# Performance work log

Hardware: AMD Instinct MI355X
Metric: run time of the kernel (lower is better)

## Reference

```python
import jax, jax.numpy as jnp
import numpy as np

B, S, N, C, D = 1, 6, 6400, 128, 4
HEADS, POINTS = 4, 20
HS, WS = 32, 88
M = HS * WS
DH = C // HEADS


def setup_inputs() -> dict:
    key = jax.random.key(0)
    ks = jax.random.split(key, 16)
    sc = 0.02
    return {
        "query": jax.random.normal(ks[0], (B, N, C), jnp.float32),
        "key": jax.random.normal(ks[1], (S, M, B, C), jnp.float32),
        "value": jax.random.normal(ks[2], (S, M, B, C), jnp.float32),
        "query_pos": jax.random.normal(ks[3], (B, N, C), jnp.float32),
        "reference_points_cam": jax.random.uniform(ks[4], (S, B, N, D, 2), jnp.float32),
        "bev_mask": jax.random.bernoulli(ks[5], 0.3, (S, B, N, D)),
        "spatial_shapes": jnp.array([[HS, WS]], jnp.int32),
        "level_start_index": jnp.zeros((1,), jnp.int32),
        "Wv": sc * jax.random.normal(ks[6], (C, C), jnp.float32),
        "bv": jnp.zeros((C,), jnp.float32),
        "Woff": sc * jax.random.normal(ks[7], (C, HEADS * POINTS * 2), jnp.float32),
        "boff": sc * jax.random.normal(ks[8], (HEADS * POINTS * 2,), jnp.float32),
        "Wattn": sc * jax.random.normal(ks[9], (C, HEADS * POINTS), jnp.float32),
        "battn": jnp.zeros((HEADS * POINTS,), jnp.float32),
        "Wout": sc * jax.random.normal(ks[10], (C, C), jnp.float32),
        "bout": jnp.zeros((C,), jnp.float32),
    }


def _bilinear(img, x, y):
    # img: (G, HS, WS, DH); x, y: (G, Q, P) pixel coords (grid_sample align_corners=False, zero padding)
    G = img.shape[0]
    flat = img.reshape(G, HS * WS, DH)
    x0 = jnp.floor(x)
    y0 = jnp.floor(y)
    wx1 = x - x0
    wy1 = y - y0
    x0i = x0.astype(jnp.int32)
    y0i = y0.astype(jnp.int32)

    def gather(xi, yi):
        valid = ((xi >= 0) & (xi < WS) & (yi >= 0) & (yi < HS)).astype(img.dtype)
        idx = jnp.clip(yi, 0, HS - 1) * WS + jnp.clip(xi, 0, WS - 1)
        v = jnp.take_along_axis(flat, idx.reshape(G, -1, 1), axis=1)
        return v.reshape(*idx.shape, DH) * valid[..., None]

    v00 = gather(x0i, y0i)
    v01 = gather(x0i + 1, y0i)
    v10 = gather(x0i, y0i + 1)
    v11 = gather(x0i + 1, y0i + 1)
    return (v00 * ((1 - wx1) * (1 - wy1))[..., None]
            + v01 * (wx1 * (1 - wy1))[..., None]
            + v10 * ((1 - wx1) * wy1)[..., None]
            + v11 * (wx1 * wy1)[..., None])


def _deform_attn(q, v, ref, spatial_shapes, Wv, bv, Woff, boff, Wattn, battn):
    # q: (bs, nq, C); v: (bs, M, C); ref: (bs, nq, D, 2) in [0,1]
    bs, nq, _ = q.shape
    val = (v @ Wv + bv).reshape(bs, HS, WS, HEADS, DH)
    val = val.transpose(0, 3, 1, 2, 4).reshape(bs * HEADS, HS, WS, DH)
    # sampling offsets, normalized by (W, H), split points into POINTS//D groups per Z-anchor
    norm = jnp.stack([spatial_shapes[0, 1], spatial_shapes[0, 0]]).astype(q.dtype)  # [W, H]
    off = (q @ Woff + boff).reshape(bs, nq, HEADS, POINTS // D, D, 2) / norm
    loc = ref[:, :, None, None, :, :] + off  # (bs, nq, HEADS, P//D, D, 2)
    loc = loc.reshape(bs, nq, HEADS, POINTS, 2).transpose(0, 2, 1, 3, 4)
    loc = loc.reshape(bs * HEADS, nq, POINTS, 2)
    x = loc[..., 0] * WS - 0.5
    y = loc[..., 1] * HS - 0.5
    sampled = _bilinear(val, x, y)  # (bs*HEADS, nq, POINTS, DH)
    aw = jax.nn.softmax((q @ Wattn + battn).reshape(bs, nq, HEADS, POINTS), axis=-1)
    aw = aw.transpose(0, 2, 1, 3).reshape(bs * HEADS, nq, POINTS)
    out = jnp.einsum('gnpd,gnp->gnd', sampled, aw)
    return out.reshape(bs, HEADS, nq, DH).transpose(0, 2, 1, 3).reshape(bs, nq, C)


def reference(query, key, value, query_pos, reference_points_cam, bev_mask,
              spatial_shapes, level_start_index,
              Wv, bv, Woff, boff, Wattn, battn, Wout, bout):
    residual = query
    q = query + query_pos
    # camera routing mask (original derives indexes from batch 0 of bev_mask)
    mask0 = (bev_mask[:, 0].sum(-1) > 0).astype(q.dtype)  # (S, N)
    # dense masked equivalent of gather/pad/attend/scatter-add: deformable attn is
    # per-query independent, so computing all queries per camera and masking is exact.
    qs = jnp.broadcast_to(q[:, None], (B, S, N, C)).reshape(B * S, N, C)
    vs = value.transpose(2, 0, 1, 3).reshape(B * S, M, C)
    refs = reference_points_cam.transpose(1, 0, 2, 3, 4).reshape(B * S, N, D, 2)
    out = _deform_attn(qs, vs, refs, spatial_shapes, Wv, bv, Woff, boff, Wattn, battn)
    out = out.reshape(B, S, N, C)
    slots = (out * mask0[None, :, :, None]).sum(1)  # (B, N, C)
    count = (bev_mask.sum(-1) > 0).astype(q.dtype).transpose(1, 2, 0).sum(-1)  # (B, N)
    slots = slots / jnp.maximum(count, 1.0)[..., None]
    slots = slots @ Wout + bout
    return slots + residual  # dropout is identity in eval
```

## Files before the change

kernel.cpp:

```cpp
#include <hip/hip_runtime.h>

#define SC 6
#define NQ 6400
#define CH 128
#define HSY 32
#define WSX 88
#define MV 2816
#define NH 4
#define NP 20
#define DD 4
#define DHC 32
#define NPG 5
#define NPAIR (SC * NH * NP)

#define NB_QPROJ 800
#define NB_VPROJ 1056
#define NB_MEGA  (1 + NB_QPROJ + NB_VPROJ)

#define WS_QOFF     38464
#define WS_AW       1062464
#define WS_VAL      1574464

__device__ __forceinline__ unsigned short f32_to_bf16(float x) {
    unsigned int u = __float_as_uint(x);
    unsigned int r = (u + 0x7FFFu + ((u >> 16) & 1u)) >> 16;
    return (unsigned short)r;
}

#define QB 8
__global__ __launch_bounds__(256) void k_mega(
        const unsigned int* __restrict__ bm,
        const float* __restrict__ q, const float* __restrict__ qpos,
        const float* __restrict__ Woff, const float* __restrict__ boff,
        const float* __restrict__ Wattn, const float* __restrict__ battn,
        const float* __restrict__ value, const float* __restrict__ Wv,
        const float* __restrict__ bv,
        int* __restrict__ flag, float* __restrict__ qoff,
        float* __restrict__ aw, unsigned short* __restrict__ valw) {
    __shared__ __align__(16) float smem[2048];
    int bid = blockIdx.x;
    int t = threadIdx.x;

    if (bid == 0) {
        unsigned int* r_or = (unsigned int*)smem;
        unsigned int* r_vi = r_or + 256;
        unsigned int o = 0u, v = 0u;
        for (int i = t; i < 2048; i += 256) {
            unsigned int w = bm[i];
            o |= (w & 0xFFFFFF00u);
            v |= (unsigned int)((w != 0u) & (w != 0x3F800000u));
        }
        r_or[t] = o; r_vi[t] = v;
        __syncthreads();
        for (int s = 128; s > 0; s >>= 1) {
            if (t < s) { r_or[t] |= r_or[t + s]; r_vi[t] |= r_vi[t + s]; }
            __syncthreads();
        }
        if (t == 0) {
            int f;
            if (!r_vi[0]) f = 2;
            else if (r_or[0]) f = 1;
            else f = 0;
            *flag = f;
        }
        return;
    }

    if (bid <= NB_QPROJ) {
        float (*qs)[QB] = (float(*)[QB])smem;
        float (*lg)[NH * NP] = (float(*)[NH * NP])(smem + CH * QB);
        int n0 = (bid - 1) * QB;
        for (int i = t; i < QB * CH; i += 256) {
            int qi = i >> 7, k = i & 127;
            int gi = (n0 + qi) * CH + k;
            qs[k][qi] = q[gi] + qpos[gi];
        }
        __syncthreads();
        if (t < 160) {
            float acc[QB];
#pragma unroll
            for (int qi = 0; qi < QB; ++qi) acc[qi] = 0.f;
            for (int k = 0; k < CH; ++k) {
                float w = Woff[k * 160 + t];
                float4 a = *(const float4*)&qs[k][0];
                float4 b = *(const float4*)&qs[k][4];
                acc[0] += a.x * w; acc[1] += a.y * w; acc[2] += a.z * w; acc[3] += a.w * w;
                acc[4] += b.x * w; acc[5] += b.y * w; acc[6] += b.z * w; acc[7] += b.w * w;
            }
            float b = boff[t];
#pragma unroll
            for (int qi = 0; qi < QB; ++qi) qoff[(n0 + qi) * 160 + t] = acc[qi] + b;
        } else if (t < 240) {
            int j = t - 160;
            float acc[QB];
#pragma unroll
            for (int qi = 0; qi < QB; ++qi) acc[qi] = 0.f;
            for (int k = 0; k < CH; ++k) {
                float w = Wattn[k * 80 + j];
                float4 a = *(const float4*)&qs[k][0];
                float4 b = *(const float4*)&qs[k][4];
                acc[0] += a.x * w; acc[1] += a.y * w; acc[2] += a.z * w; acc[3] += a.w * w;
                acc[4] += b.x * w; acc[5] += b.y * w; acc[6] += b.z * w; acc[7] += b.w * w;
            }
            float b = battn[j];
#pragma unroll
            for (int qi = 0; qi < QB; ++qi) lg[qi][j] = acc[qi] + b;
        }
        __syncthreads();
        if (t < QB * NH) {
            int qi = t >> 2, h = t & 3;
            float mx = -1e30f;
#pragma unroll
            for (int p = 0; p < NP; ++p) mx = fmaxf(mx, lg[qi][h * NP + p]);
            float e[NP];
            float sm = 0.f;
#pragma unroll
            for (int p = 0; p < NP; ++p) { e[p] = __expf(lg[qi][h * NP + p] - mx); sm += e[p]; }
            float inv = 1.f / sm;
#pragma unroll
            for (int p = 0; p < NP; ++p) aw[(n0 + qi) * 80 + h * NP + p] = e[p] * inv;
        }
        return;
    }

    {
        float (*vs)[16] = (float(*)[16])smem;
        int r0 = (bid - 1 - NB_QPROJ) * 16;
        for (int i = t; i < 16 * CH; i += 256) {
            int ri = i >> 7, k = i & 127;
            vs[k][ri] = value[(size_t)(r0 + ri) * CH + k];
        }
        __syncthreads();
        int c = t & 127, rh = t >> 7;
        float acc[8];
#pragma unroll
        for (int ri = 0; ri < 8; ++ri) acc[ri] = 0.f;
        for (int k = 0; k < CH; ++k) {
            float w = Wv[k * CH + c];
            float4 a = *(const float4*)&vs[k][rh * 8];
            float4 b = *(const float4*)&vs[k][rh * 8 + 4];
            acc[0] += a.x * w; acc[1] += a.y * w; acc[2] += a.z * w; acc[3] += a.w * w;
            acc[4] += b.x * w; acc[5] += b.y * w; acc[6] += b.z * w; acc[7] += b.w * w;
        }
        float b = bv[c];
        int h = c >> 5, dh = c & 31;
#pragma unroll
        for (int ri = 0; ri < 8; ++ri) {
            int r = r0 + rh * 8 + ri;
            int s = r / MV;
            int m = r - s * MV;
            valw[(size_t)((s * NH + h) * MV + m) * DHC + dh] = f32_to_bf16(acc[ri] + b);
        }
    }
}

#define REDP 36
__global__ __launch_bounds__(320) void k_sample2(
        const float* __restrict__ ref, const float* __restrict__ qoff,
        const float* __restrict__ aw, const void* __restrict__ bm,
        const int* __restrict__ flag, const unsigned short* __restrict__ valw,
        const float* __restrict__ Wout, const float* __restrict__ bout,
        const float* __restrict__ query, float* __restrict__ out) {
    int bid = blockIdx.x;
    int pi = (bid & 7) * (NQ / 16) + (bid >> 3);
    int n0 = pi * 2;
    int t = threadIdx.x;

    __shared__ float qo[2][160];
    __shared__ float awl[2][NH * NP];
    __shared__ float rf[2][SC][DD][2];
    __shared__ float mk[2][SC];
    __shared__ int   pairI[NPAIR][4];
    __shared__ float pairW[NPAIR][4];
    __shared__ float red[80][REDP];
    __shared__ float sl[2][CH];

    {
        int qq = t / 160, idx = t - qq * 160;
        qo[qq][idx] = qoff[(size_t)(n0 + qq) * 160 + idx];
    }
    if (t < 160) {
        int qq = t / 80, idx = t - qq * 80;
        awl[qq][idx] = aw[(size_t)(n0 + qq) * 80 + idx];
    }
    if (t >= 160 && t < 256) {
        int i = t - 160;
        int qq = i / 48, rem = i - qq * 48;
        int s = rem >> 3, r2 = rem & 7;
        rf[qq][s][r2 >> 1][r2 & 1] = ref[(size_t)(s * NQ + n0 + qq) * 8 + r2];
    }
    if (t >= 256 && t < 256 + 2 * SC) {
        int i = t - 256;
        int qq = i / SC, s = i - qq * SC;
        int gi = s * NQ + n0 + qq;
        int f = *flag;
        int any;
        if (f == 1) {
            const unsigned char* p = (const unsigned char*)bm + (size_t)gi * 4;
            any = (int)(p[0] | p[1] | p[2] | p[3]);
        } else if (f == 0) {
            const int* p = (const int*)bm + (size_t)gi * 4;
            any = p[0] | p[1] | p[2] | p[3];
        } else {
            const float* p = (const float*)bm + (size_t)gi * 4;
            any = (p[0] != 0.f) | (p[1] != 0.f) | (p[2] != 0.f) | (p[3] != 0.f);
        }
        mk[qq][s] = any ? 1.0f : 0.0f;
    }
    __syncthreads();

    for (int qq = 0; qq < 2; ++qq) {
        for (int i = t; i < NPAIR; i += 320) {
            int s = i / (NH * NP);
            int q = i - s * (NH * NP);
            int h = q & 3;
            int p = q >> 2;
            int g = p >> 2, d = p & 3;
            float x = rf[qq][s][d][0] * (float)WSX + qo[qq][((h * NPG + g) * DD + d) * 2 + 0] - 0.5f;
            float y = rf[qq][s][d][1] * (float)HSY + qo[qq][((h * NPG + g) * DD + d) * 2 + 1] - 0.5f;
            float xf = floorf(x), yf = floorf(y);
            float wx = x - xf, wy = y - yf;
            int x0 = (int)xf, y0 = (int)yf;
            int x1 = x0 + 1, y1 = y0 + 1;
            float vx0 = (x0 >= 0 && x0 < WSX) ? 1.f : 0.f;
            float vx1 = (x1 >= 0 && x1 < WSX) ? 1.f : 0.f;
            float vy0 = (y0 >= 0 && y0 < HSY) ? 1.f : 0.f;
            float vy1 = (y1 >= 0 && y1 < HSY) ? 1.f : 0.f;
            int cx0 = min(max(x0, 0), WSX - 1), cx1 = min(max(x1, 0), WSX - 1);
            int cy0 = min(max(y0, 0), HSY - 1), cy1 = min(max(y1, 0), HSY - 1);
            int base = (s * NH + h) * MV;
            pairI[i][0] = (base + cy0 * WSX + cx0) * DHC;
            pairI[i][1] = (base + cy0 * WSX + cx1) * DHC;
            pairI[i][2] = (base + cy1 * WSX + cx0) * DHC;
            pairI[i][3] = (base + cy1 * WSX + cx1) * DHC;
            float a = awl[qq][h * NP + p];
            pairW[i][0] = (1.f - wx) * (1.f - wy) * vx0 * vy0 * a;
            pairW[i][1] = wx * (1.f - wy) * vx1 * vy0 * a;
            pairW[i][2] = (1.f - wx) * wy * vx0 * vy1 * a;
            pairW[i][3] = wx * wy * vx1 * vy1 * a;
        }
        __syncthreads();

        int sid = t >> 2;
        int c8 = t & 3;
        int coff = c8 * 8;
        float acc[8];
#pragma unroll
        for (int j = 0; j < 8; ++j) acc[j] = 0.f;
        for (int s = 0; s < SC; ++s) {
            if (mk[qq][s] == 0.f) continue;
            int pr = s * (NH * NP) + sid;
            int4  ii = *(const int4*)pairI[pr];
            float4 ww = *(const float4*)pairW[pr];
#define CORNER(IDX, W)  {                                              \
            uint4 u = *(const uint4*)(valw + (IDX) + coff);            \
            float w_ = (W);                                            \
            acc[0] += w_ * __uint_as_float(u.x << 16);                 \
            acc[1] += w_ * __uint_as_float(u.x & 0xFFFF0000u);         \
            acc[2] += w_ * __uint_as_float(u.y << 16);                 \
            acc[3] += w_ * __uint_as_float(u.y & 0xFFFF0000u);         \
            acc[4] += w_ * __uint_as_float(u.z << 16);                 \
            acc[5] += w_ * __uint_as_float(u.z & 0xFFFF0000u);         \
            acc[6] += w_ * __uint_as_float(u.w << 16);                 \
            acc[7] += w_ * __uint_as_float(u.w & 0xFFFF0000u);         \
        }
            CORNER(ii.x, ww.x)
            CORNER(ii.y, ww.y)
            CORNER(ii.z, ww.z)
            CORNER(ii.w, ww.w)
#undef CORNER
        }
        *(float4*)&red[sid][coff] = make_float4(acc[0], acc[1], acc[2], acc[3]);
        *(float4*)&red[sid][coff + 4] = make_float4(acc[4], acc[5], acc[6], acc[7]);
        __syncthreads();

        if (t < CH) {
            int h = t >> 5, ch = t & 31;
            float sum = 0.f;
#pragma unroll
            for (int p = 0; p < NP; ++p) sum += red[p * 4 + h][ch];
            float cnt = mk[qq][0] + mk[qq][1] + mk[qq][2] + mk[qq][3] + mk[qq][4] + mk[qq][5];
            sl[qq][t] = sum / fmaxf(cnt, 1.0f);
        }
        __syncthreads();
    }

    if (t < 256) {
        int c = t & 127;
        int qq = t >> 7;
        float acc = 0.f;
        for (int k = 0; k < CH; ++k) acc += sl[qq][k] * Wout[k * CH + c];
        int gi = (n0 + qq) * CH + c;
        out[gi] = acc + bout[c] + query[gi];
    }
}

extern "C" void kernel_launch(void* const* d_in, const int* in_sizes, int n_in,
                              void* d_out, int out_size, void* d_ws, size_t ws_size,
                              hipStream_t stream) {
    const float* query     = (const float*)d_in[0];
    const float* value     = (const float*)d_in[2];
    const float* query_pos = (const float*)d_in[3];
    const float* refcam    = (const float*)d_in[4];
    const void*  bev_mask  = (const void*)d_in[5];
    const float* Wv    = (const float*)d_in[8];
    const float* bv    = (const float*)d_in[9];
    const float* Woff  = (const float*)d_in[10];
    const float* boff  = (const float*)d_in[11];
    const float* Wattn = (const float*)d_in[12];
    const float* battn = (const float*)d_in[13];
    const float* Wout  = (const float*)d_in[14];
    const float* bout  = (const float*)d_in[15];

    float* wsf   = (float*)d_ws;
    int*   flag  = (int*)d_ws;
    float* qoff  = wsf + WS_QOFF;
    float* aw    = wsf + WS_AW;
    unsigned short* valw = (unsigned short*)(wsf + WS_VAL);
    float* out   = (float*)d_out;

    k_mega<<<NB_MEGA, 256, 0, stream>>>((const unsigned int*)bev_mask,
                                        query, query_pos, Woff, boff, Wattn, battn,
                                        value, Wv, bv, flag, qoff, aw, valw);
    k_sample2<<<NQ / 2, 320, 0, stream>>>(refcam, qoff, aw, bev_mask, flag, valw,
                                          Wout, bout, query, out);
}
```

Measured before the change: 164.3 us.

## Compute bilinear sample indices in registers and process both queries in one pass

The sampling kernel no longer builds per-pair corner index and weight tables in shared memory. Each thread now computes its bilinear coordinates and weights inline and accumulates both queries of the block in one loop over cameras, which removes several block barriers and the shared-memory round trip. The projection stage also gets larger tiles (16 queries and 32 value rows per block) for more register reuse of weights, and writes bf16 values with a simpler address computation. Costs are higher register pressure and more address arithmetic per thread, plus corner loads issued for a camera whenever either query is masked in.

```diff
diff --git a/kernel.cpp b/kernel.cpp
--- a/kernel.cpp
+++ b/kernel.cpp
@@ -11,10 +11,11 @@
 #define DD 4
 #define DHC 32
 #define NPG 5
-#define NPAIR (SC * NH * NP)
-
-#define NB_QPROJ 800
-#define NB_VPROJ 1056
+
+#define QB2 16
+#define VB2 32
+#define NB_QPROJ (NQ / QB2)
+#define NB_VPROJ (SC * MV / VB2)
 #define NB_MEGA  (1 + NB_QPROJ + NB_VPROJ)
 
 #define WS_QOFF     38464
@@ -27,7 +28,6 @@
     return (unsigned short)r;
 }
 
-#define QB 8
 __global__ __launch_bounds__(256) void k_mega(
         const unsigned int* __restrict__ bm,
         const float* __restrict__ q, const float* __restrict__ qpos,
@@ -37,7 +37,7 @@
         const float* __restrict__ bv,
         int* __restrict__ flag, float* __restrict__ qoff,
         float* __restrict__ aw, unsigned short* __restrict__ valw) {
-    __shared__ __align__(16) float smem[2048];
+    __shared__ __align__(16) float smem[4096 + QB2 * NH * NP];
     int bid = blockIdx.x;
     int t = threadIdx.x;
 
@@ -67,47 +67,51 @@
     }
 
     if (bid <= NB_QPROJ) {
-        float (*qs)[QB] = (float(*)[QB])smem;
-        float (*lg)[NH * NP] = (float(*)[NH * NP])(smem + CH * QB);
-        int n0 = (bid - 1) * QB;
-        for (int i = t; i < QB * CH; i += 256) {
+        float (*qs)[QB2] = (float(*)[QB2])smem;
+        float (*lg)[NH * NP] = (float(*)[NH * NP])(smem + 4096);
+        int n0 = (bid - 1) * QB2;
+        for (int i = t; i < QB2 * CH; i += 256) {
             int qi = i >> 7, k = i & 127;
             int gi = (n0 + qi) * CH + k;
             qs[k][qi] = q[gi] + qpos[gi];
         }
         __syncthreads();
         if (t < 160) {
-            float acc[QB];
-#pragma unroll
-            for (int qi = 0; qi < QB; ++qi) acc[qi] = 0.f;
+            float acc[QB2];
+#pragma unroll
+            for (int qi = 0; qi < QB2; ++qi) acc[qi] = 0.f;
             for (int k = 0; k < CH; ++k) {
                 float w = Woff[k * 160 + t];
-                float4 a = *(const float4*)&qs[k][0];
-                float4 b = *(const float4*)&qs[k][4];
-                acc[0] += a.x * w; acc[1] += a.y * w; acc[2] += a.z * w; acc[3] += a.w * w;
-                acc[4] += b.x * w; acc[5] += b.y * w; acc[6] += b.z * w; acc[7] += b.w * w;
+#pragma unroll
+                for (int v4 = 0; v4 < QB2 / 4; ++v4) {
+                    float4 a = *(const float4*)&qs[k][v4 * 4];
+                    acc[v4 * 4 + 0] += a.x * w; acc[v4 * 4 + 1] += a.y * w;
+                    acc[v4 * 4 + 2] += a.z * w; acc[v4 * 4 + 3] += a.w * w;
+                }
             }
             float b = boff[t];
 #pragma unroll
-            for (int qi = 0; qi < QB; ++qi) qoff[(n0 + qi) * 160 + t] = acc[qi] + b;
+            for (int qi = 0; qi < QB2; ++qi) qoff[(n0 + qi) * 160 + t] = acc[qi] + b;
         } else if (t < 240) {
             int j = t - 160;
-            float acc[QB];
-#pragma unroll
-            for (int qi = 0; qi < QB; ++qi) acc[qi] = 0.f;
+            float acc[QB2];
+#pragma unroll
+            for (int qi = 0; qi < QB2; ++qi) acc[qi] = 0.f;
             for (int k = 0; k < CH; ++k) {
                 float w = Wattn[k * 80 + j];
-                float4 a = *(const float4*)&qs[k][0];
-                float4 b = *(const float4*)&qs[k][4];
-                acc[0] += a.x * w; acc[1] += a.y * w; acc[2] += a.z * w; acc[3] += a.w * w;
-                acc[4] += b.x * w; acc[5] += b.y * w; acc[6] += b.z * w; acc[7] += b.w * w;
+#pragma unroll
+                for (int v4 = 0; v4 < QB2 / 4; ++v4) {
+                    float4 a = *(const float4*)&qs[k][v4 * 4];
+                    acc[v4 * 4 + 0] += a.x * w; acc[v4 * 4 + 1] += a.y * w;
+                    acc[v4 * 4 + 2] += a.z * w; acc[v4 * 4 + 3] += a.w * w;
+                }
             }
             float b = battn[j];
 #pragma unroll
-            for (int qi = 0; qi < QB; ++qi) lg[qi][j] = acc[qi] + b;
+            for (int qi = 0; qi < QB2; ++qi) lg[qi][j] = acc[qi] + b;
         }
         __syncthreads();
-        if (t < QB * NH) {
+        if (t < QB2 * NH) {
             int qi = t >> 2, h = t & 3;
             float mx = -1e30f;
 #pragma unroll
@@ -124,38 +128,40 @@
     }
 
     {
-        float (*vs)[16] = (float(*)[16])smem;
-        int r0 = (bid - 1 - NB_QPROJ) * 16;
-        for (int i = t; i < 16 * CH; i += 256) {
-            int ri = i >> 7, k = i & 127;
+        float (*vs)[VB2] = (float(*)[VB2])smem;
+        int r0 = (bid - 1 - NB_QPROJ) * VB2;
+        for (int i = t; i < VB2 * CH; i += 256) {
+            int ri = i & (VB2 - 1), k = i / VB2;
             vs[k][ri] = value[(size_t)(r0 + ri) * CH + k];
         }
         __syncthreads();
         int c = t & 127, rh = t >> 7;
-        float acc[8];
-#pragma unroll
-        for (int ri = 0; ri < 8; ++ri) acc[ri] = 0.f;
+        float acc[16];
+#pragma unroll
+        for (int ri = 0; ri < 16; ++ri) acc[ri] = 0.f;
         for (int k = 0; k < CH; ++k) {
             float w = Wv[k * CH + c];
-            float4 a = *(const float4*)&vs[k][rh * 8];
-            float4 b = *(const float4*)&vs[k][rh * 8 + 4];
-            acc[0] += a.x * w; acc[1] += a.y * w; acc[2] += a.z * w; acc[3] += a.w * w;
-            acc[4] += b.x * w; acc[5] += b.y * w; acc[6] += b.z * w; acc[7] += b.w * w;
+#pragma unroll
+            for (int v4 = 0; v4 < 4; ++v4) {
+                float4 a = *(const float4*)&vs[k][rh * 16 + v4 * 4];
+                acc[v4 * 4 + 0] += a.x * w; acc[v4 * 4 + 1] += a.y * w;
+                acc[v4 * 4 + 2] += a.z * w; acc[v4 * 4 + 3] += a.w * w;
+            }
         }
         float b = bv[c];
         int h = c >> 5, dh = c & 31;
-#pragma unroll
-        for (int ri = 0; ri < 8; ++ri) {
-            int r = r0 + rh * 8 + ri;
-            int s = r / MV;
-            int m = r - s * MV;
-            valw[(size_t)((s * NH + h) * MV + m) * DHC + dh] = f32_to_bf16(acc[ri] + b);
+        int s = r0 / MV;
+        int m0 = r0 - s * MV + rh * 16;
+        size_t obase = (size_t)((s * NH + h) * MV) * DHC + dh;
+#pragma unroll
+        for (int ri = 0; ri < 16; ++ri) {
+            valw[obase + (size_t)(m0 + ri) * DHC] = f32_to_bf16(acc[ri] + b);
         }
     }
 }
 
 #define REDP 36
-__global__ __launch_bounds__(320) void k_sample2(
+__global__ __launch_bounds__(320) void k_sample3(
         const float* __restrict__ ref, const float* __restrict__ qoff,
         const float* __restrict__ aw, const void* __restrict__ bm,
         const int* __restrict__ flag, const unsigned short* __restrict__ valw,
@@ -170,9 +176,7 @@
     __shared__ float awl[2][NH * NP];
     __shared__ float rf[2][SC][DD][2];
     __shared__ float mk[2][SC];
-    __shared__ int   pairI[NPAIR][4];
-    __shared__ float pairW[NPAIR][4];
-    __shared__ float red[80][REDP];
+    __shared__ float red[2][80][REDP];
     __shared__ float sl[2][CH];
 
     {
@@ -209,85 +213,90 @@
     }
     __syncthreads();
 
-    for (int qq = 0; qq < 2; ++qq) {
-        for (int i = t; i < NPAIR; i += 320) {
-            int s = i / (NH * NP);
-            int q = i - s * (NH * NP);
-            int h = q & 3;
-            int p = q >> 2;
-            int g = p >> 2, d = p & 3;
-            float x = rf[qq][s][d][0] * (float)WSX + qo[qq][((h * NPG + g) * DD + d) * 2 + 0] - 0.5f;
-            float y = rf[qq][s][d][1] * (float)HSY + qo[qq][((h * NPG + g) * DD + d) * 2 + 1] - 0.5f;
-            float xf = floorf(x), yf = floorf(y);
-            float wx = x - xf, wy = y - yf;
-            int x0 = (int)xf, y0 = (int)yf;
-            int x1 = x0 + 1, y1 = y0 + 1;
-            float vx0 = (x0 >= 0 && x0 < WSX) ? 1.f : 0.f;
-            float vx1 = (x1 >= 0 && x1 < WSX) ? 1.f : 0.f;
-            float vy0 = (y0 >= 0 && y0 < HSY) ? 1.f : 0.f;
-            float vy1 = (y1 >= 0 && y1 < HSY) ? 1.f : 0.f;
-            int cx0 = min(max(x0, 0), WSX - 1), cx1 = min(max(x1, 0), WSX - 1);
-            int cy0 = min(max(y0, 0), HSY - 1), cy1 = min(max(y1, 0), HSY - 1);
-            int base = (s * NH + h) * MV;
-            pairI[i][0] = (base + cy0 * WSX + cx0) * DHC;
-            pairI[i][1] = (base + cy0 * WSX + cx1) * DHC;
-            pairI[i][2] = (base + cy1 * WSX + cx0) * DHC;
-            pairI[i][3] = (base + cy1 * WSX + cx1) * DHC;
-            float a = awl[qq][h * NP + p];
-            pairW[i][0] = (1.f - wx) * (1.f - wy) * vx0 * vy0 * a;
-            pairW[i][1] = wx * (1.f - wy) * vx1 * vy0 * a;
-            pairW[i][2] = (1.f - wx) * wy * vx0 * vy1 * a;
-            pairW[i][3] = wx * wy * vx1 * vy1 * a;
-        }
-        __syncthreads();
-
-        int sid = t >> 2;
-        int c8 = t & 3;
-        int coff = c8 * 8;
-        float acc[8];
-#pragma unroll
-        for (int j = 0; j < 8; ++j) acc[j] = 0.f;
-        for (int s = 0; s < SC; ++s) {
-            if (mk[qq][s] == 0.f) continue;
-            int pr = s * (NH * NP) + sid;
-            int4  ii = *(const int4*)pairI[pr];
-            float4 ww = *(const float4*)pairW[pr];
-#define CORNER(IDX, W)  {                                              \
-            uint4 u = *(const uint4*)(valw + (IDX) + coff);            \
-            float w_ = (W);                                            \
-            acc[0] += w_ * __uint_as_float(u.x << 16);                 \
-            acc[1] += w_ * __uint_as_float(u.x & 0xFFFF0000u);         \
-            acc[2] += w_ * __uint_as_float(u.y << 16);                 \
-            acc[3] += w_ * __uint_as_float(u.y & 0xFFFF0000u);         \
-            acc[4] += w_ * __uint_as_float(u.z << 16);                 \
-            acc[5] += w_ * __uint_as_float(u.z & 0xFFFF0000u);         \
-            acc[6] += w_ * __uint_as_float(u.w << 16);                 \
-            acc[7] += w_ * __uint_as_float(u.w & 0xFFFF0000u);         \
-        }
-            CORNER(ii.x, ww.x)
-            CORNER(ii.y, ww.y)
-            CORNER(ii.z, ww.z)
-            CORNER(ii.w, ww.w)
-#undef CORNER
-        }
-        *(float4*)&red[sid][coff] = make_float4(acc[0], acc[1], acc[2], acc[3]);
-        *(float4*)&red[sid][coff + 4] = make_float4(acc[4], acc[5], acc[6], acc[7]);
-        __syncthreads();
-
-        if (t < CH) {
-            int h = t >> 5, ch = t & 31;
-            float sum = 0.f;
-#pragma unroll
-            for (int p = 0; p < NP; ++p) sum += red[p * 4 + h][ch];
-            float cnt = mk[qq][0] + mk[qq][1] + mk[qq][2] + mk[qq][3] + mk[qq][4] + mk[qq][5];
-            sl[qq][t] = sum / fmaxf(cnt, 1.0f);
-        }
-        __syncthreads();
-    }
+    int sid = t >> 2;
+    int c8 = t & 3;
+    int coff = c8 * 8;
+    int h = sid & 3, p = sid >> 2;
+    int g = p >> 2, d = p & 3;
+    int oidx = ((h * NPG + g) * DD + d) * 2;
+    float qox0 = qo[0][oidx], qoy0 = qo[0][oidx + 1];
+    float qox1 = qo[1][oidx], qoy1 = qo[1][oidx + 1];
+    float aw0 = awl[0][h * NP + p], aw1 = awl[1][h * NP + p];
+
+    float acc0[8], acc1[8];
+#pragma unroll
+    for (int j = 0; j < 8; ++j) { acc0[j] = 0.f; acc1[j] = 0.f; }
+
+#define SAMPLE_Q(ACC, RFX, RFY, QOX, QOY, AWQ, MKQ)  {                         \
+        float x = (RFX) * (float)WSX + (QOX) - 0.5f;                           \
+        float y = (RFY) * (float)HSY + (QOY) - 0.5f;                           \
+        float xf = floorf(x), yf = floorf(y);                                  \
+        float wx = x - xf, wy = y - yf;                                        \
+        int x0 = (int)xf, y0 = (int)yf;                                        \
+        int x1 = x0 + 1, y1 = y0 + 1;                                          \
+        float vx0 = (x0 >= 0 && x0 < WSX) ? 1.f : 0.f;                         \
+        float vx1 = (x1 >= 0 && x1 < WSX) ? 1.f : 0.f;                         \
+        float vy0 = (y0 >= 0 && y0 < HSY) ? 1.f : 0.f;                         \
+        float vy1 = (y1 >= 0 && y1 < HSY) ? 1.f : 0.f;                         \
+        int cx0 = min(max(x0, 0), WSX - 1), cx1 = min(max(x1, 0), WSX - 1);    \
+        int cy0 = min(max(y0, 0), HSY - 1), cy1 = min(max(y1, 0), HSY - 1);    \
+        float a_ = (AWQ) * (MKQ);                                              \
+        float w00 = (1.f - wx) * (1.f - wy) * vx0 * vy0 * a_;                  \
+        float w01 = wx * (1.f - wy) * vx1 * vy0 * a_;                          \
+        float w10 = (1.f - wx) * wy * vx0 * vy1 * a_;                          \
+        float w11 = wx * wy * vx1 * vy1 * a_;                                  \
+        const unsigned short* vb = valw + (size_t)base_s * DHC + coff;         \
+        uint4 u00 = *(const uint4*)(vb + (cy0 * WSX + cx0) * DHC);             \
+        uint4 u01 = *(const uint4*)(vb + (cy0 * WSX + cx1) * DHC);             \
+        uint4 u10 = *(const uint4*)(vb + (cy1 * WSX + cx0) * DHC);             \
+        uint4 u11 = *(const uint4*)(vb + (cy1 * WSX + cx1) * DHC);             \
+        ACC[0] += w00 * __uint_as_float(u00.x << 16) + w01 * __uint_as_float(u01.x << 16)          \
+                + w10 * __uint_as_float(u10.x << 16) + w11 * __uint_as_float(u11.x << 16);         \
+        ACC[1] += w00 * __uint_as_float(u00.x & 0xFFFF0000u) + w01 * __uint_as_float(u01.x & 0xFFFF0000u)  \
+                + w10 * __uint_as_float(u10.x & 0xFFFF0000u) + w11 * __uint_as_float(u11.x & 0xFFFF0000u); \
+        ACC[2] += w00 * __uint_as_float(u00.y << 16) + w01 * __uint_as_float(u01.y << 16)          \
+                + w10 * __uint_as_float(u10.y << 16) + w11 * __uint_as_float(u11.y << 16);         \
+        ACC[3] += w00 * __uint_as_float(u00.y & 0xFFFF0000u) + w01 * __uint_as_float(u01.y & 0xFFFF0000u)  \
+                + w10 * __uint_as_float(u10.y & 0xFFFF0000u) + w11 * __uint_as_float(u11.y & 0xFFFF0000u); \
+        ACC[4] += w00 * __uint_as_float(u00.z << 16) + w01 * __uint_as_float(u01.z << 16)          \
+                + w10 * __uint_as_float(u10.z << 16) + w11 * __uint_as_float(u11.z << 16);         \
+        ACC[5] += w00 * __uint_as_float(u00.z & 0xFFFF0000u) + w01 * __uint_as_float(u01.z & 0xFFFF0000u)  \
+                + w10 * __uint_as_float(u10.z & 0xFFFF0000u) + w11 * __uint_as_float(u11.z & 0xFFFF0000u); \
+        ACC[6] += w00 * __uint_as_float(u00.w << 16) + w01 * __uint_as_float(u01.w << 16)          \
+                + w10 * __uint_as_float(u10.w << 16) + w11 * __uint_as_float(u11.w << 16);         \
+        ACC[7] += w00 * __uint_as_float(u00.w & 0xFFFF0000u) + w01 * __uint_as_float(u01.w & 0xFFFF0000u)  \
+                + w10 * __uint_as_float(u10.w & 0xFFFF0000u) + w11 * __uint_as_float(u11.w & 0xFFFF0000u); \
+    }
+
+#pragma unroll
+    for (int s = 0; s < SC; ++s) {
+        float m0 = mk[0][s], m1 = mk[1][s];
+        if (m0 == 0.f && m1 == 0.f) continue;
+        int base_s = (s * NH + h) * MV;
+        SAMPLE_Q(acc0, rf[0][s][d][0], rf[0][s][d][1], qox0, qoy0, aw0, m0)
+        SAMPLE_Q(acc1, rf[1][s][d][0], rf[1][s][d][1], qox1, qoy1, aw1, m1)
+    }
+#undef SAMPLE_Q
+
+    *(float4*)&red[0][sid][coff]     = make_float4(acc0[0], acc0[1], acc0[2], acc0[3]);
+    *(float4*)&red[0][sid][coff + 4] = make_float4(acc0[4], acc0[5], acc0[6], acc0[7]);
+    *(float4*)&red[1][sid][coff]     = make_float4(acc1[0], acc1[1], acc1[2], acc1[3]);
+    *(float4*)&red[1][sid][coff + 4] = make_float4(acc1[4], acc1[5], acc1[6], acc1[7]);
+    __syncthreads();
 
     if (t < 256) {
-        int c = t & 127;
-        int qq = t >> 7;
+        int qq = t >> 7, c = t & 127;
+        int hh = c >> 5, ch = c & 31;
+        float sum = 0.f;
+#pragma unroll
+        for (int p2 = 0; p2 < NP; ++p2) sum += red[qq][p2 * 4 + hh][ch];
+        float cnt = mk[qq][0] + mk[qq][1] + mk[qq][2] + mk[qq][3] + mk[qq][4] + mk[qq][5];
+        sl[qq][c] = sum / fmaxf(cnt, 1.0f);
+    }
+    __syncthreads();
+
+    if (t < 256) {
+        int qq = t >> 7, c = t & 127;
         float acc = 0.f;
         for (int k = 0; k < CH; ++k) acc += sl[qq][k] * Wout[k * CH + c];
         int gi = (n0 + qq) * CH + c;
@@ -322,6 +331,6 @@
     k_mega<<<NB_MEGA, 256, 0, stream>>>((const unsigned int*)bev_mask,
                                         query, query_pos, Woff, boff, Wattn, battn,
                                         value, Wv, bv, flag, qoff, aw, valw);
-    k_sample2<<<NQ / 2, 320, 0, stream>>>(refcam, qoff, aw, bev_mask, flag, valw,
+    k_sample3<<<NQ / 2, 320, 0, stream>>>(refcam, qoff, aw, bev_mask, flag, valw,
                                           Wout, bout, query, out);
 }
```

Result: slower. 185.4 us (+12.9%).

## Stage projection weights in LDS with larger row tiles and packed sample FMAs

Applied to the files above, without the earlier changes.

The query-offset and value projection phases of the mega kernel now process twice as many rows per block (16 queries, 32 value rows) and stage the weight matrices through shared memory in 32-row K chunks, instead of reading weights from global memory per row. This raises weight reuse and halves the block count, at the cost of much larger shared-memory use (about 43 KB) and more registers, which may lower occupancy. The value output index is now computed once per block on the assumption that a tile never crosses a camera boundary. The sampling kernel's bilinear accumulation is rewritten with float2 math to encourage packed FMA instructions.

```diff
diff --git a/kernel.cpp b/kernel.cpp
--- a/kernel.cpp
+++ b/kernel.cpp
@@ -13,8 +13,10 @@
 #define NPG 5
 #define NPAIR (SC * NH * NP)
 
-#define NB_QPROJ 800
-#define NB_VPROJ 1056
+#define QB2 16
+#define VB2 32
+#define NB_QPROJ (NQ / QB2)
+#define NB_VPROJ (SC * MV / VB2)
 #define NB_MEGA  (1 + NB_QPROJ + NB_VPROJ)
 
 #define WS_QOFF     38464
@@ -27,7 +29,6 @@
     return (unsigned short)r;
 }
 
-#define QB 8
 __global__ __launch_bounds__(256) void k_mega(
         const unsigned int* __restrict__ bm,
         const float* __restrict__ q, const float* __restrict__ qpos,
@@ -37,7 +38,7 @@
         const float* __restrict__ bv,
         int* __restrict__ flag, float* __restrict__ qoff,
         float* __restrict__ aw, unsigned short* __restrict__ valw) {
-    __shared__ __align__(16) float smem[2048];
+    __shared__ __align__(16) float smem[11008];
     int bid = blockIdx.x;
     int t = threadIdx.x;
 
@@ -67,47 +68,67 @@
     }
 
     if (bid <= NB_QPROJ) {
-        float (*qs)[QB] = (float(*)[QB])smem;
-        float (*lg)[NH * NP] = (float(*)[NH * NP])(smem + CH * QB);
-        int n0 = (bid - 1) * QB;
-        for (int i = t; i < QB * CH; i += 256) {
+        float (*qs)[QB2] = (float(*)[QB2])smem;
+        float* wst = smem + 2048;
+        float (*lg)[NH * NP] = (float(*)[NH * NP])(smem + 9728);
+        int n0 = (bid - 1) * QB2;
+        for (int i = t; i < QB2 * CH; i += 256) {
             int qi = i >> 7, k = i & 127;
             int gi = (n0 + qi) * CH + k;
             qs[k][qi] = q[gi] + qpos[gi];
         }
-        __syncthreads();
+        float acc[QB2];
+#pragma unroll
+        for (int qi = 0; qi < QB2; ++qi) acc[qi] = 0.f;
+
+        for (int kc = 0; kc < 4; ++kc) {
+            for (int j = t; j < 5120; j += 256) {
+                int kk = j / 160, cc = j - kk * 160;
+                wst[j] = Woff[(kc * 32 + kk) * 160 + cc];
+            }
+            for (int j = t; j < 2560; j += 256) {
+                int kk = j / 80, cc = j - kk * 80;
+                wst[5120 + j] = Wattn[(kc * 32 + kk) * 80 + cc];
+            }
+            __syncthreads();
+            if (t < 160) {
+                for (int kk = 0; kk < 32; ++kk) {
+                    float w = wst[kk * 160 + t];
+                    const float* qrow = &qs[kc * 32 + kk][0];
+#pragma unroll
+                    for (int v4 = 0; v4 < QB2 / 4; ++v4) {
+                        float4 a = *(const float4*)(qrow + v4 * 4);
+                        acc[v4 * 4 + 0] += a.x * w; acc[v4 * 4 + 1] += a.y * w;
+                        acc[v4 * 4 + 2] += a.z * w; acc[v4 * 4 + 3] += a.w * w;
+                    }
+                }
+            } else if (t < 240) {
+                int j = t - 160;
+                for (int kk = 0; kk < 32; ++kk) {
+                    float w = wst[5120 + kk * 80 + j];
+                    const float* qrow = &qs[kc * 32 + kk][0];
+#pragma unroll
+                    for (int v4 = 0; v4 < QB2 / 4; ++v4) {
+                        float4 a = *(const float4*)(qrow + v4 * 4);
+                        acc[v4 * 4 + 0] += a.x * w; acc[v4 * 4 + 1] += a.y * w;
+                        acc[v4 * 4 + 2] += a.z * w; acc[v4 * 4 + 3] += a.w * w;
+                    }
+                }
+            }
+            __syncthreads();
+        }
         if (t < 160) {
-            float acc[QB];
-#pragma unroll
-            for (int qi = 0; qi < QB; ++qi) acc[qi] = 0.f;
-            for (int k = 0; k < CH; ++k) {
-                float w = Woff[k * 160 + t];
-                float4 a = *(const float4*)&qs[k][0];
-                float4 b = *(const float4*)&qs[k][4];
-                acc[0] += a.x * w; acc[1] += a.y * w; acc[2] += a.z * w; acc[3] += a.w * w;
-                acc[4] += b.x * w; acc[5] += b.y * w; acc[6] += b.z * w; acc[7] += b.w * w;
-            }
             float b = boff[t];
 #pragma unroll
-            for (int qi = 0; qi < QB; ++qi) qoff[(n0 + qi) * 160 + t] = acc[qi] + b;
+            for (int qi = 0; qi < QB2; ++qi) qoff[(n0 + qi) * 160 + t] = acc[qi] + b;
         } else if (t < 240) {
             int j = t - 160;
-            float acc[QB];
-#pragma unroll
-            for (int qi = 0; qi < QB; ++qi) acc[qi] = 0.f;
-            for (int k = 0; k < CH; ++k) {
-                float w = Wattn[k * 80 + j];
-                float4 a = *(const float4*)&qs[k][0];
-                float4 b = *(const float4*)&qs[k][4];
-                acc[0] += a.x * w; acc[1] += a.y * w; acc[2] += a.z * w; acc[3] += a.w * w;
-                acc[4] += b.x * w; acc[5] += b.y * w; acc[6] += b.z * w; acc[7] += b.w * w;
-            }
             float b = battn[j];
 #pragma unroll
-            for (int qi = 0; qi < QB; ++qi) lg[qi][j] = acc[qi] + b;
-        }
-        __syncthreads();
-        if (t < QB * NH) {
+            for (int qi = 0; qi < QB2; ++qi) lg[qi][j] = acc[qi] + b;
+        }
+        __syncthreads();
+        if (t < QB2 * NH) {
             int qi = t >> 2, h = t & 3;
             float mx = -1e30f;
 #pragma unroll
@@ -124,32 +145,43 @@
     }
 
     {
-        float (*vs)[16] = (float(*)[16])smem;
-        int r0 = (bid - 1 - NB_QPROJ) * 16;
-        for (int i = t; i < 16 * CH; i += 256) {
+        float* vs = smem;
+        float* wvt = smem + 4608;
+        int r0 = (bid - 1 - NB_QPROJ) * VB2;
+        for (int i = t; i < VB2 * CH; i += 256) {
             int ri = i >> 7, k = i & 127;
-            vs[k][ri] = value[(size_t)(r0 + ri) * CH + k];
-        }
-        __syncthreads();
+            vs[k * 36 + ri] = value[(size_t)(r0 + ri) * CH + k];
+        }
         int c = t & 127, rh = t >> 7;
-        float acc[8];
-#pragma unroll
-        for (int ri = 0; ri < 8; ++ri) acc[ri] = 0.f;
-        for (int k = 0; k < CH; ++k) {
-            float w = Wv[k * CH + c];
-            float4 a = *(const float4*)&vs[k][rh * 8];
-            float4 b = *(const float4*)&vs[k][rh * 8 + 4];
-            acc[0] += a.x * w; acc[1] += a.y * w; acc[2] += a.z * w; acc[3] += a.w * w;
-            acc[4] += b.x * w; acc[5] += b.y * w; acc[6] += b.z * w; acc[7] += b.w * w;
+        float acc[16];
+#pragma unroll
+        for (int ri = 0; ri < 16; ++ri) acc[ri] = 0.f;
+
+        for (int kc = 0; kc < 4; ++kc) {
+            for (int j = t; j < 4096; j += 256) {
+                wvt[j] = Wv[(kc * 32 + (j >> 7)) * 128 + (j & 127)];
+            }
+            __syncthreads();
+            for (int kk = 0; kk < 32; ++kk) {
+                float w = wvt[kk * 128 + c];
+                const float* vrow = vs + (kc * 32 + kk) * 36 + rh * 16;
+#pragma unroll
+                for (int v4 = 0; v4 < 4; ++v4) {
+                    float4 a = *(const float4*)(vrow + v4 * 4);
+                    acc[v4 * 4 + 0] += a.x * w; acc[v4 * 4 + 1] += a.y * w;
+                    acc[v4 * 4 + 2] += a.z * w; acc[v4 * 4 + 3] += a.w * w;
+                }
+            }
+            __syncthreads();
         }
         float b = bv[c];
         int h = c >> 5, dh = c & 31;
-#pragma unroll
-        for (int ri = 0; ri < 8; ++ri) {
-            int r = r0 + rh * 8 + ri;
-            int s = r / MV;
-            int m = r - s * MV;
-            valw[(size_t)((s * NH + h) * MV + m) * DHC + dh] = f32_to_bf16(acc[ri] + b);
+        int s = r0 / MV;
+        int m0 = r0 - s * MV + rh * 16;
+        size_t obase = (size_t)((s * NH + h) * MV) * DHC + dh;
+#pragma unroll
+        for (int ri = 0; ri < 16; ++ri) {
+            valw[obase + (size_t)(m0 + ri) * DHC] = f32_to_bf16(acc[ri] + b);
         }
     }
 }
@@ -244,25 +276,28 @@
         int sid = t >> 2;
         int c8 = t & 3;
         int coff = c8 * 8;
-        float acc[8];
-#pragma unroll
-        for (int j = 0; j < 8; ++j) acc[j] = 0.f;
+        float2 acc2[4];
+#pragma unroll
+        for (int j = 0; j < 4; ++j) acc2[j] = make_float2(0.f, 0.f);
         for (int s = 0; s < SC; ++s) {
             if (mk[qq][s] == 0.f) continue;
             int pr = s * (NH * NP) + sid;
             int4  ii = *(const int4*)pairI[pr];
             float4 ww = *(const float4*)pairW[pr];
-#define CORNER(IDX, W)  {                                              \
-            uint4 u = *(const uint4*)(valw + (IDX) + coff);            \
-            float w_ = (W);                                            \
-            acc[0] += w_ * __uint_as_float(u.x << 16);                 \
-            acc[1] += w_ * __uint_as_float(u.x & 0xFFFF0000u);         \
-            acc[2] += w_ * __uint_as_float(u.y << 16);                 \
-            acc[3] += w_ * __uint_as_float(u.y & 0xFFFF0000u);         \
-            acc[4] += w_ * __uint_as_float(u.z << 16);                 \
-            acc[5] += w_ * __uint_as_float(u.z & 0xFFFF0000u);         \
-            acc[6] += w_ * __uint_as_float(u.w << 16);                 \
-            acc[7] += w_ * __uint_as_float(u.w & 0xFFFF0000u);         \
+#define CORNER(IDX, W)  {                                                     \
+            uint4 u = *(const uint4*)(valw + (IDX) + coff);                   \
+            float w_ = (W);                                                   \
+            float2 w2 = make_float2(w_, w_);                                  \
+            float2 f0 = make_float2(__uint_as_float(u.x << 16),               \
+                                    __uint_as_float(u.x & 0xFFFF0000u));      \
+            float2 f1 = make_float2(__uint_as_float(u.y << 16),               \
+                                    __uint_as_float(u.y & 0xFFFF0000u));      \
+            float2 f2 = make_float2(__uint_as_float(u.z << 16),               \
+                                    __uint_as_float(u.z & 0xFFFF0000u));      \
+            float2 f3 = make_float2(__uint_as_float(u.w << 16),               \
+                                    __uint_as_float(u.w & 0xFFFF0000u));      \
+            acc2[0] += w2 * f0; acc2[1] += w2 * f1;                           \
+            acc2[2] += w2 * f2; acc2[3] += w2 * f3;                           \
         }
             CORNER(ii.x, ww.x)
             CORNER(ii.y, ww.y)
@@ -270,8 +305,8 @@
             CORNER(ii.w, ww.w)
 #undef CORNER
         }
-        *(float4*)&red[sid][coff] = make_float4(acc[0], acc[1], acc[2], acc[3]);
-        *(float4*)&red[sid][coff + 4] = make_float4(acc[4], acc[5], acc[6], acc[7]);
+        *(float4*)&red[sid][coff]     = make_float4(acc2[0].x, acc2[0].y, acc2[1].x, acc2[1].y);
+        *(float4*)&red[sid][coff + 4] = make_float4(acc2[2].x, acc2[2].y, acc2[3].x, acc2[3].y);
         __syncthreads();
 
         if (t < CH) {
```

Result: slower. 186.8 us (+13.7%).
